# Optimization experiments

Hardware: AMD Instinct MI355X
Metric: run time of the kernel (lower is better)

The kernel has to match this reference:

```python
import jax, jax.numpy as jnp
import numpy as np

B, T, D = 4, 2048, 1024
DEPTH = 4
LEAF_DIM = 256
NUM_LEAVES = 2 ** DEPTH          # 16
NUM_NODES = NUM_LEAVES - 1       # 15


def _uniform(key, shape, scale):
    s = 1.0 / np.sqrt(scale)
    return jax.random.uniform(key, shape, minval=-s, maxval=s, dtype=jnp.float32)


def setup_inputs() -> dict:
    key = jax.random.key(0)
    ks = jax.random.split(key, 8)
    x = jax.random.normal(ks[0], (B, T, D), dtype=jnp.float32)
    # gate params: Dense(1) per internal node, level-order layout
    node_w = _uniform(ks[1], (NUM_NODES, D), D)
    node_b = _uniform(ks[2], (NUM_NODES,), D)
    # leaf MLP params: D -> LEAF_DIM -> D, stacked over leaves
    w1 = _uniform(ks[3], (NUM_LEAVES, D, LEAF_DIM), D)
    b1 = _uniform(ks[4], (NUM_LEAVES, LEAF_DIM), D)
    w2 = _uniform(ks[5], (NUM_LEAVES, LEAF_DIM, D), LEAF_DIM)
    b2 = _uniform(ks[6], (NUM_LEAVES, D), LEAF_DIM)
    return {"x": x, "node_w": node_w, "node_b": node_b,
            "w1": w1, "b1": b1, "w2": w2, "b2": b2, "training": 0}


def _leaf_probs(x, node_w, node_b, depth):
    # gate activations for all internal nodes at once: [B,T,NUM_NODES]
    c = jax.nn.sigmoid(jnp.einsum('btd,nd->btn', x, node_w) + node_b)
    probs = jnp.ones(c.shape[:-1] + (1,), dtype=c.dtype)
    for m in range(depth):
        start = 2 ** m - 1
        cl = c[..., start:start + 2 ** m]          # gates at level m: [B,T,2^m]
        # left child gets c, right child gets (1-c); interleave preserves
        # the recursion's n -> (2n, 2n+1) indexing
        probs = jnp.stack([probs * cl, probs * (1.0 - cl)], axis=-1)
        probs = probs.reshape(probs.shape[:-2] + (-1,))
    return probs                                   # [B,T,NUM_LEAVES]


def reference(x, node_w, node_b, w1, b1, w2, b2, training):
    num_leaves = w1.shape[0]
    depth = int(np.log2(num_leaves))
    probs = _leaf_probs(x, node_w, node_b, depth)          # [B,T,L]
    # all leaf MLP hidden layers as one batched GEMM
    h = jax.nn.relu(jnp.einsum('btd,ldh->btlh', x, w1) + b1)
    # weight hidden by leaf probability, then contract l and h together so the
    # [B,T,L,D] per-leaf output is never materialized
    h = h * probs[..., None]
    out = jnp.einsum('btlh,lhd->btd', h, w2)
    out = out + jnp.einsum('btl,ld->btd', probs, b2)
    return out
```

## Files before the change

kernel.cpp:

```cpp
#include <hip/hip_runtime.h>
#include <stdint.h>

typedef unsigned short ushort_t;
typedef __bf16 bf16x8 __attribute__((ext_vector_type(8)));
typedef float f32x4 __attribute__((ext_vector_type(4)));

#define M_TOK 8192
#define K1 1024
#define N1 4096
#define K2 4160
#define N2 1024

#define SGB(m, n) __builtin_amdgcn_sched_group_barrier((m), (n), 0)
#define SGB_DS   0x100
#define SGB_MFMA 0x008

__device__ __forceinline__ ushort_t f2bf(float f) {
  union { float f; unsigned u; } v; v.f = f;
  unsigned u = v.u;
  u += 0x7FFFu + ((u >> 16) & 1u);
  return (ushort_t)(u >> 16);
}

__device__ __forceinline__ void gload16(const void* g, void* l) {
  __builtin_amdgcn_global_load_lds((__attribute__((address_space(1))) void*)g,
                                   (__attribute__((address_space(3))) void*)l,
                                   16, 0, 0);
}

__global__ __launch_bounds__(256) void k_probs(
    const float* __restrict__ x, const float* __restrict__ node_w,
    const float* __restrict__ node_b, ushort_t* __restrict__ xb,
    float* __restrict__ probs, ushort_t* __restrict__ hp) {
  const int wid = threadIdx.x >> 6, lane = threadIdx.x & 63;
  const int t = blockIdx.x * 4 + wid;
  const float* xr = x + (size_t)t * K1;
  float xv[16];
#pragma unroll
  for (int j = 0; j < 4; ++j) {
    float4 v = *(const float4*)(xr + j * 256 + lane * 4);
    xv[4*j+0] = v.x; xv[4*j+1] = v.y; xv[4*j+2] = v.z; xv[4*j+3] = v.w;
  }
  ushort_t* xbr = xb + (size_t)t * K1;
#pragma unroll
  for (int j = 0; j < 4; ++j) {
    ushort4 o;
    o.x = f2bf(xv[4*j+0]); o.y = f2bf(xv[4*j+1]);
    o.z = f2bf(xv[4*j+2]); o.w = f2bf(xv[4*j+3]);
    *(ushort4*)(xbr + j * 256 + lane * 4) = o;
  }
  float c[15];
#pragma unroll
  for (int n = 0; n < 15; ++n) {
    float s = 0.f;
    const float* wr = node_w + n * K1;
#pragma unroll
    for (int j = 0; j < 4; ++j) {
      float4 w = *(const float4*)(wr + j * 256 + lane * 4);
      s += xv[4*j+0]*w.x + xv[4*j+1]*w.y + xv[4*j+2]*w.z + xv[4*j+3]*w.w;
    }
#pragma unroll
    for (int off = 32; off > 0; off >>= 1) s += __shfl_xor(s, off);
    float z = s + node_b[n];
    c[n] = 1.f / (1.f + __expf(-z));
  }
  if (lane < 16) {
    float p = 1.f;
#pragma unroll
    for (int m = 0; m < 4; ++m) {
      int jm = lane >> (4 - m);
      int node = (1 << m) - 1 + jm;
      int bit = (lane >> (3 - m)) & 1;
      p *= bit ? (1.f - c[node]) : c[node];
    }
    probs[t * 16 + lane] = p;
    hp[(size_t)t * K2 + 4096 + lane] = f2bf(p);
  }
  if (lane < 48) hp[(size_t)t * K2 + 4112 + lane] = 0;
}

__global__ __launch_bounds__(256) void k_wprep(
    const float* __restrict__ w1, const float* __restrict__ w2,
    const float* __restrict__ b2, ushort_t* __restrict__ w1t,
    ushort_t* __restrict__ w2t) {
  __shared__ ushort_t tile[64][68];
  const int b = blockIdx.x;
  const int tr = threadIdx.x >> 4;
  const int tc = (threadIdx.x & 15) * 4;
  if (b < 1024) {
    const int l = b >> 6, rem = b & 63;
    const int kt = rem >> 2, ht = rem & 3;
    const float* in = w1 + (size_t)l * K1 * 256;
#pragma unroll
    for (int rr = 0; rr < 4; ++rr) {
      int r = tr + rr * 16;
      float4 v = *(const float4*)(in + (size_t)(kt * 64 + r) * 256 + ht * 64 + tc);
      tile[r][tc+0] = f2bf(v.x); tile[r][tc+1] = f2bf(v.y);
      tile[r][tc+2] = f2bf(v.z); tile[r][tc+3] = f2bf(v.w);
    }
    __syncthreads();
#pragma unroll
    for (int rr = 0; rr < 4; ++rr) {
      int oh = tr + rr * 16;
      ushort4 o;
      o.x = tile[tc+0][oh]; o.y = tile[tc+1][oh];
      o.z = tile[tc+2][oh]; o.w = tile[tc+3][oh];
      *(ushort4*)(w1t + (size_t)(l * 256 + ht * 64 + oh) * K1 + kt * 64 + tc) = o;
    }
  } else if (b < 2048) {
    const int bb = b - 1024;
    const int l = bb >> 6, rem = bb & 63;
    const int ht = rem >> 4, dt = rem & 15;
    const float* in = w2 + (size_t)l * 256 * N2;
#pragma unroll
    for (int rr = 0; rr < 4; ++rr) {
      int r = tr + rr * 16;
      float4 v = *(const float4*)(in + (size_t)(ht * 64 + r) * N2 + dt * 64 + tc);
      tile[r][tc+0] = f2bf(v.x); tile[r][tc+1] = f2bf(v.y);
      tile[r][tc+2] = f2bf(v.z); tile[r][tc+3] = f2bf(v.w);
    }
    __syncthreads();
#pragma unroll
    for (int rr = 0; rr < 4; ++rr) {
      int od = tr + rr * 16;
      ushort4 o;
      o.x = tile[tc+0][od]; o.y = tile[tc+1][od];
      o.z = tile[tc+2][od]; o.w = tile[tc+3][od];
      *(ushort4*)(w2t + (size_t)(dt * 64 + od) * K2 + l * 256 + ht * 64 + tc) = o;
    }
  } else {
    int tid = (b - 2048) * 256 + threadIdx.x;
    int d = tid >> 6, cc = tid & 63;
    float v = (cc < 16) ? b2[cc * N2 + d] : 0.f;
    w2t[(size_t)d * K2 + 4096 + cc] = f2bf(v);
  }
}

template <int NT, int LDA, int LDB, int BN, int MODE>
__global__ __launch_bounds__(512, 2) void k_gemm8(
    const ushort_t* __restrict__ A, const ushort_t* __restrict__ Bt,
    const float* __restrict__ probs, const float* __restrict__ b1,
    ushort_t* __restrict__ hp, float* __restrict__ out, int ntn) {
  constexpr int BHR = BN / 2;
  constexpr int WN = (BN == 256) ? 4 : 2;
  constexpr int WM = 8 / WN;
  constexpr int FH = 128 / (WM * 16);
  constexpr int ABYTES = 128 * 128;
  constexpr int BBYTES = BHR * 128;
  constexpr int KEEP = 2 + 2 * (BHR / 64);

  extern __shared__ char lds[];
  const int tid = threadIdx.x;
  int bid = blockIdx.x;
  const int nwg = gridDim.x;
  bid = (bid & 7) * (nwg >> 3) + (bid >> 3);
  const int bm = bid / ntn, bn = bid % ntn;

  const int wid = tid >> 6, lane = tid & 63;
  const int widM = wid / WN, widN = wid % WN;
  const int wmBase = widM * (FH * 16);
  const int wn = widN * 64;
  const int lr = lane & 15, g = lane >> 4;

  const ushort_t* Ag = A + (size_t)bm * 256 * LDA;
  const ushort_t* Bg = Bt + (size_t)bn * BN * LDB;

  const int srow = tid >> 3;
  const int scol = ((tid & 7) << 4) ^ ((srow & 7) << 4);

  auto stageA = [&](int buf, int half, int kt) {
    const ushort_t* src = Ag + (size_t)(half * 128) * LDA + kt * 64;
    char* dst = lds + (buf * 2 + half) * ABYTES + tid * 16;
#pragma unroll
    for (int r = 0; r < 2; ++r)
      gload16((const char*)(src + (size_t)(srow + r * 64) * LDA) + scol,
              dst + r * 8192);
  };
  auto stageB = [&](int buf, int half, int kt) {
    const ushort_t* src = Bg + (size_t)(half * BHR) * LDB + kt * 64;
    char* dst = lds + 4 * ABYTES + (buf * 2 + half) * BBYTES + tid * 16;
#pragma unroll
    for (int r = 0; r < BHR / 64; ++r)
      gload16((const char*)(src + (size_t)(srow + r * 64) * LDB) + scol,
              dst + r * 8192);
  };
  auto rdA = [&](int buf, int half, int i, int kk) -> bf16x8 {
    int r = wmBase + i * 16 + lr;
    int off = r * 128 + (((kk * 4 + g) ^ (lr & 7)) << 4);
    return *(const bf16x8*)(lds + (buf * 2 + half) * ABYTES + off);
  };
  auto rdB = [&](int buf, int j, int kk) -> bf16x8 {
    int nr = wn + j * 16;
    int half = (nr >= BHR) ? 1 : 0;
    int r = (nr & (BHR - 1)) + lr;
    int off = r * 128 + (((kk * 4 + g) ^ (lr & 7)) << 4);
    return *(const bf16x8*)(lds + 4 * ABYTES + (buf * 2 + half) * BBYTES + off);
  };

  f32x4 acc[2 * FH][4];
#pragma unroll
  for (int i = 0; i < 2 * FH; ++i)
#pragma unroll
    for (int j = 0; j < 4; ++j) acc[i][j] = (f32x4){0.f, 0.f, 0.f, 0.f};

  stageA(0, 0, 0); stageA(0, 1, 0); stageB(0, 0, 0); stageB(0, 1, 0);
  stageA(1, 0, 1); stageB(1, 0, 1); stageB(1, 1, 1);
  if constexpr (KEEP == 6) asm volatile("s_waitcnt vmcnt(6)" ::: "memory");
  else                     asm volatile("s_waitcnt vmcnt(4)" ::: "memory");
  __builtin_amdgcn_sched_barrier(0);
  __builtin_amdgcn_s_barrier();
  __builtin_amdgcn_sched_barrier(0);

#pragma unroll 1
  for (int kt = 0; kt < NT; ++kt) {
    const int cur = kt & 1;
    bf16x8 bfr[2][4];

    {
      bf16x8 a0[FH][2];
#pragma unroll
      for (int kk = 0; kk < 2; ++kk) {
#pragma unroll
        for (int i = 0; i < FH; ++i) a0[i][kk] = rdA(cur, 0, i, kk);
#pragma unroll
        for (int j = 0; j < 4; ++j) bfr[kk][j] = rdB(cur, j, kk);
      }
      if (kt + 1 < NT) stageA(cur ^ 1, 1, kt + 1);
      __builtin_amdgcn_s_setprio(1);
#pragma unroll
      for (int kk = 0; kk < 2; ++kk)
#pragma unroll
        for (int j = 0; j < 4; ++j)
#pragma unroll
          for (int i = 0; i < FH; ++i)
            acc[i][j] = __builtin_amdgcn_mfma_f32_16x16x32_bf16(
                a0[i][kk], bfr[kk][j], acc[i][j], 0, 0, 0);
      __builtin_amdgcn_s_setprio(0);
#pragma unroll
      for (int kk = 0; kk < 2; ++kk) {
        SGB(SGB_DS, FH + 1); SGB(SGB_MFMA, FH);
#pragma unroll
        for (int rep = 0; rep < 3; ++rep) { SGB(SGB_DS, 1); SGB(SGB_MFMA, FH); }
      }
    }
    __builtin_amdgcn_s_barrier();
    __builtin_amdgcn_sched_barrier(0);

    {
      bf16x8 a1[FH][2];
#pragma unroll
      for (int kk = 0; kk < 2; ++kk)
#pragma unroll
        for (int i = 0; i < FH; ++i) a1[i][kk] = rdA(cur, 1, i, kk);
      if (kt + 2 < NT) {
        stageA(cur, 0, kt + 2);
        stageB(cur, 0, kt + 2);
        stageB(cur, 1, kt + 2);
      }
      __builtin_amdgcn_s_setprio(1);
#pragma unroll
      for (int kk = 0; kk < 2; ++kk)
#pragma unroll
        for (int j = 0; j < 4; ++j)
#pragma unroll
          for (int i = 0; i < FH; ++i)
            acc[FH + i][j] = __builtin_amdgcn_mfma_f32_16x16x32_bf16(
                a1[i][kk], bfr[kk][j], acc[FH + i][j], 0, 0, 0);
      __builtin_amdgcn_s_setprio(0);
#pragma unroll
      for (int kk = 0; kk < 2; ++kk) {
        SGB(SGB_DS, FH); SGB(SGB_MFMA, 2 * FH); SGB(SGB_MFMA, 2 * FH);
      }
    }
    if (kt + 2 < NT) {
      if constexpr (KEEP == 6) asm volatile("s_waitcnt vmcnt(6)" ::: "memory");
      else                     asm volatile("s_waitcnt vmcnt(4)" ::: "memory");
      __builtin_amdgcn_sched_barrier(0);
    } else if (kt + 1 < NT) {
      asm volatile("s_waitcnt vmcnt(0)" ::: "memory");
      __builtin_amdgcn_sched_barrier(0);
    }
    __builtin_amdgcn_s_barrier();
    __builtin_amdgcn_sched_barrier(0);
  }

  const int rowb = bm * 256 + wmBase + g * 4;
  const int colb = bn * BN + wn + lr;
  if (MODE == 0) {
    const int leaf = bn;
#pragma unroll
    for (int q = 0; q < 2; ++q)
#pragma unroll
      for (int i = 0; i < FH; ++i) {
        int rbase = rowb + q * 128 + i * 16;
        float pm[4];
#pragma unroll
        for (int rg = 0; rg < 4; ++rg)
          pm[rg] = probs[(size_t)(rbase + rg) * 16 + leaf];
#pragma unroll
        for (int j = 0; j < 4; ++j) {
          float bias = b1[colb + j * 16];
#pragma unroll
          for (int rg = 0; rg < 4; ++rg) {
            float v = acc[q * FH + i][j][rg] + bias;
            v = v > 0.f ? v : 0.f;
            v *= pm[rg];
            hp[(size_t)(rbase + rg) * K2 + colb + j * 16] = f2bf(v);
          }
        }
      }
  } else {
#pragma unroll
    for (int q = 0; q < 2; ++q)
#pragma unroll
      for (int i = 0; i < FH; ++i) {
        int rbase = rowb + q * 128 + i * 16;
#pragma unroll
        for (int j = 0; j < 4; ++j)
#pragma unroll
          for (int rg = 0; rg < 4; ++rg)
            out[(size_t)(rbase + rg) * N2 + colb + j * 16] = acc[q * FH + i][j][rg];
      }
  }
}

extern "C" void kernel_launch(void* const* d_in, const int* in_sizes, int n_in,
                              void* d_out, int out_size, void* d_ws, size_t ws_size,
                              hipStream_t stream) {
  const float* x      = (const float*)d_in[0];
  const float* node_w = (const float*)d_in[1];
  const float* node_b = (const float*)d_in[2];
  const float* w1     = (const float*)d_in[3];
  const float* b1     = (const float*)d_in[4];
  const float* w2     = (const float*)d_in[5];
  const float* b2     = (const float*)d_in[6];
  float* out = (float*)d_out;

  char* ws = (char*)d_ws;
  ushort_t* xb    = (ushort_t*)(ws);
  ushort_t* w1t   = (ushort_t*)(ws + 16777216);
  ushort_t* w2t   = (ushort_t*)(ws + 25165824);
  ushort_t* hp    = (ushort_t*)(ws + 33685504);
  float*    probs = (float*)   (ws + 101842944);

  k_probs<<<M_TOK / 4, 256, 0, stream>>>(x, node_w, node_b, xb, probs, hp);
  k_wprep<<<2304, 256, 0, stream>>>(w1, w2, b2, w1t, w2t);
  k_gemm8<16, K1, K1, 256, 0><<<512, 512, 131072, stream>>>(
      xb, w1t, probs, b1, hp, nullptr, N1 / 256);
  k_gemm8<65, K2, K2, 128, 1><<<256, 512, 98304, stream>>>(
      hp, w2t, nullptr, nullptr, nullptr, out, N2 / 128);
}
```

Before: 179.3 us.

## Merge prep kernels, unroll GEMM k-loop by two, precompute staging pointers

The gate/probability kernel and the weight-transpose kernel become one launch with a larger grid, removing a kernel launch and its gap. In the GEMM, the per-lane global source pointers are computed once, so each stage only adds an offset. The k-loop is unrolled by two with a compile-time buffer index, which makes LDS offsets constant. The explicit sched_group_barrier interleaving hints are removed, so instruction interleaving is left to the compiler and may get worse.

```diff
diff --git a/kernel.cpp b/kernel.cpp
--- a/kernel.cpp
+++ b/kernel.cpp
@@ -11,9 +11,7 @@
 #define K2 4160
 #define N2 1024
 
-#define SGB(m, n) __builtin_amdgcn_sched_group_barrier((m), (n), 0)
-#define SGB_DS   0x100
-#define SGB_MFMA 0x008
+template <int V> struct ic { static constexpr int value = V; };
 
 __device__ __forceinline__ ushort_t f2bf(float f) {
   union { float f; unsigned u; } v; v.f = f;
@@ -28,66 +26,17 @@
                                    16, 0, 0);
 }
 
-__global__ __launch_bounds__(256) void k_probs(
+__global__ __launch_bounds__(256) void k_prep(
     const float* __restrict__ x, const float* __restrict__ node_w,
-    const float* __restrict__ node_b, ushort_t* __restrict__ xb,
-    float* __restrict__ probs, ushort_t* __restrict__ hp) {
-  const int wid = threadIdx.x >> 6, lane = threadIdx.x & 63;
-  const int t = blockIdx.x * 4 + wid;
-  const float* xr = x + (size_t)t * K1;
-  float xv[16];
-#pragma unroll
-  for (int j = 0; j < 4; ++j) {
-    float4 v = *(const float4*)(xr + j * 256 + lane * 4);
-    xv[4*j+0] = v.x; xv[4*j+1] = v.y; xv[4*j+2] = v.z; xv[4*j+3] = v.w;
-  }
-  ushort_t* xbr = xb + (size_t)t * K1;
-#pragma unroll
-  for (int j = 0; j < 4; ++j) {
-    ushort4 o;
-    o.x = f2bf(xv[4*j+0]); o.y = f2bf(xv[4*j+1]);
-    o.z = f2bf(xv[4*j+2]); o.w = f2bf(xv[4*j+3]);
-    *(ushort4*)(xbr + j * 256 + lane * 4) = o;
-  }
-  float c[15];
-#pragma unroll
-  for (int n = 0; n < 15; ++n) {
-    float s = 0.f;
-    const float* wr = node_w + n * K1;
-#pragma unroll
-    for (int j = 0; j < 4; ++j) {
-      float4 w = *(const float4*)(wr + j * 256 + lane * 4);
-      s += xv[4*j+0]*w.x + xv[4*j+1]*w.y + xv[4*j+2]*w.z + xv[4*j+3]*w.w;
-    }
-#pragma unroll
-    for (int off = 32; off > 0; off >>= 1) s += __shfl_xor(s, off);
-    float z = s + node_b[n];
-    c[n] = 1.f / (1.f + __expf(-z));
-  }
-  if (lane < 16) {
-    float p = 1.f;
-#pragma unroll
-    for (int m = 0; m < 4; ++m) {
-      int jm = lane >> (4 - m);
-      int node = (1 << m) - 1 + jm;
-      int bit = (lane >> (3 - m)) & 1;
-      p *= bit ? (1.f - c[node]) : c[node];
-    }
-    probs[t * 16 + lane] = p;
-    hp[(size_t)t * K2 + 4096 + lane] = f2bf(p);
-  }
-  if (lane < 48) hp[(size_t)t * K2 + 4112 + lane] = 0;
-}
-
-__global__ __launch_bounds__(256) void k_wprep(
-    const float* __restrict__ w1, const float* __restrict__ w2,
-    const float* __restrict__ b2, ushort_t* __restrict__ w1t,
-    ushort_t* __restrict__ w2t) {
+    const float* __restrict__ node_b, const float* __restrict__ w1,
+    const float* __restrict__ w2, const float* __restrict__ b2,
+    ushort_t* __restrict__ xb, float* __restrict__ probs,
+    ushort_t* __restrict__ w1t, ushort_t* __restrict__ w2t,
+    ushort_t* __restrict__ hp) {
   __shared__ ushort_t tile[64][68];
   const int b = blockIdx.x;
-  const int tr = threadIdx.x >> 4;
-  const int tc = (threadIdx.x & 15) * 4;
   if (b < 1024) {
+    const int tr = threadIdx.x >> 4, tc = (threadIdx.x & 15) * 4;
     const int l = b >> 6, rem = b & 63;
     const int kt = rem >> 2, ht = rem & 3;
     const float* in = w1 + (size_t)l * K1 * 256;
@@ -108,6 +57,7 @@
       *(ushort4*)(w1t + (size_t)(l * 256 + ht * 64 + oh) * K1 + kt * 64 + tc) = o;
     }
   } else if (b < 2048) {
+    const int tr = threadIdx.x >> 4, tc = (threadIdx.x & 15) * 4;
     const int bb = b - 1024;
     const int l = bb >> 6, rem = bb & 63;
     const int ht = rem >> 4, dt = rem & 15;
@@ -128,11 +78,57 @@
       o.z = tile[tc+2][od]; o.w = tile[tc+3][od];
       *(ushort4*)(w2t + (size_t)(dt * 64 + od) * K2 + l * 256 + ht * 64 + tc) = o;
     }
-  } else {
+  } else if (b < 2304) {
     int tid = (b - 2048) * 256 + threadIdx.x;
     int d = tid >> 6, cc = tid & 63;
     float v = (cc < 16) ? b2[cc * N2 + d] : 0.f;
     w2t[(size_t)d * K2 + 4096 + cc] = f2bf(v);
+  } else {
+    const int wid = threadIdx.x >> 6, lane = threadIdx.x & 63;
+    const int t = (b - 2304) * 4 + wid;
+    const float* xr = x + (size_t)t * K1;
+    float xv[16];
+#pragma unroll
+    for (int j = 0; j < 4; ++j) {
+      float4 v = *(const float4*)(xr + j * 256 + lane * 4);
+      xv[4*j+0] = v.x; xv[4*j+1] = v.y; xv[4*j+2] = v.z; xv[4*j+3] = v.w;
+    }
+    ushort_t* xbr = xb + (size_t)t * K1;
+#pragma unroll
+    for (int j = 0; j < 4; ++j) {
+      ushort4 o;
+      o.x = f2bf(xv[4*j+0]); o.y = f2bf(xv[4*j+1]);
+      o.z = f2bf(xv[4*j+2]); o.w = f2bf(xv[4*j+3]);
+      *(ushort4*)(xbr + j * 256 + lane * 4) = o;
+    }
+    float c[15];
+#pragma unroll
+    for (int n = 0; n < 15; ++n) {
+      float s = 0.f;
+      const float* wr = node_w + n * K1;
+#pragma unroll
+      for (int j = 0; j < 4; ++j) {
+        float4 w = *(const float4*)(wr + j * 256 + lane * 4);
+        s += xv[4*j+0]*w.x + xv[4*j+1]*w.y + xv[4*j+2]*w.z + xv[4*j+3]*w.w;
+      }
+#pragma unroll
+      for (int off = 32; off > 0; off >>= 1) s += __shfl_xor(s, off);
+      float z = s + node_b[n];
+      c[n] = 1.f / (1.f + __expf(-z));
+    }
+    if (lane < 16) {
+      float p = 1.f;
+#pragma unroll
+      for (int m = 0; m < 4; ++m) {
+        int jm = lane >> (4 - m);
+        int node = (1 << m) - 1 + jm;
+        int bit = (lane >> (3 - m)) & 1;
+        p *= bit ? (1.f - c[node]) : c[node];
+      }
+      probs[t * 16 + lane] = p;
+      hp[(size_t)t * K2 + 4096 + lane] = f2bf(p);
+    }
+    if (lane < 48) hp[(size_t)t * K2 + 4112 + lane] = 0;
   }
 }
 
@@ -168,21 +164,22 @@
   const int srow = tid >> 3;
   const int scol = ((tid & 7) << 4) ^ ((srow & 7) << 4);
 
+  const char* pA = (const char*)(Ag + (size_t)srow * LDA) + scol;
+  const char* pB = (const char*)(Bg + (size_t)srow * LDB) + scol;
+
   auto stageA = [&](int buf, int half, int kt) {
-    const ushort_t* src = Ag + (size_t)(half * 128) * LDA + kt * 64;
+    const char* src = pA + (size_t)(half * 128) * (LDA * 2) + kt * 128;
     char* dst = lds + (buf * 2 + half) * ABYTES + tid * 16;
 #pragma unroll
     for (int r = 0; r < 2; ++r)
-      gload16((const char*)(src + (size_t)(srow + r * 64) * LDA) + scol,
-              dst + r * 8192);
+      gload16(src + (size_t)(r * 64) * (LDA * 2), dst + r * 8192);
   };
   auto stageB = [&](int buf, int half, int kt) {
-    const ushort_t* src = Bg + (size_t)(half * BHR) * LDB + kt * 64;
+    const char* src = pB + (size_t)(half * BHR) * (LDB * 2) + kt * 128;
     char* dst = lds + 4 * ABYTES + (buf * 2 + half) * BBYTES + tid * 16;
 #pragma unroll
     for (int r = 0; r < BHR / 64; ++r)
-      gload16((const char*)(src + (size_t)(srow + r * 64) * LDB) + scol,
-              dst + r * 8192);
+      gload16(src + (size_t)(r * 64) * (LDB * 2), dst + r * 8192);
   };
   auto rdA = [&](int buf, int half, int i, int kk) -> bf16x8 {
     int r = wmBase + i * 16 + lr;
@@ -211,11 +208,9 @@
   __builtin_amdgcn_s_barrier();
   __builtin_amdgcn_sched_barrier(0);
 
-#pragma unroll 1
-  for (int kt = 0; kt < NT; ++kt) {
-    const int cur = kt & 1;
+  auto body = [&](auto CURC, int kt) {
+    constexpr int cur = decltype(CURC)::value;
     bf16x8 bfr[2][4];
-
     {
       bf16x8 a0[FH][2];
 #pragma unroll
@@ -236,16 +231,9 @@
             acc[i][j] = __builtin_amdgcn_mfma_f32_16x16x32_bf16(
                 a0[i][kk], bfr[kk][j], acc[i][j], 0, 0, 0);
       __builtin_amdgcn_s_setprio(0);
-#pragma unroll
-      for (int kk = 0; kk < 2; ++kk) {
-        SGB(SGB_DS, FH + 1); SGB(SGB_MFMA, FH);
-#pragma unroll
-        for (int rep = 0; rep < 3; ++rep) { SGB(SGB_DS, 1); SGB(SGB_MFMA, FH); }
-      }
     }
     __builtin_amdgcn_s_barrier();
     __builtin_amdgcn_sched_barrier(0);
-
     {
       bf16x8 a1[FH][2];
 #pragma unroll
@@ -267,10 +255,6 @@
             acc[FH + i][j] = __builtin_amdgcn_mfma_f32_16x16x32_bf16(
                 a1[i][kk], bfr[kk][j], acc[FH + i][j], 0, 0, 0);
       __builtin_amdgcn_s_setprio(0);
-#pragma unroll
-      for (int kk = 0; kk < 2; ++kk) {
-        SGB(SGB_DS, FH); SGB(SGB_MFMA, 2 * FH); SGB(SGB_MFMA, 2 * FH);
-      }
     }
     if (kt + 2 < NT) {
       if constexpr (KEEP == 6) asm volatile("s_waitcnt vmcnt(6)" ::: "memory");
@@ -282,7 +266,15 @@
     }
     __builtin_amdgcn_s_barrier();
     __builtin_amdgcn_sched_barrier(0);
+  };
+
+  int kt = 0;
+#pragma unroll 1
+  for (int it = 0; it < NT / 2; ++it) {
+    body(ic<0>{}, kt); ++kt;
+    body(ic<1>{}, kt); ++kt;
   }
+  if constexpr (NT & 1) body(ic<0>{}, kt);
 
   const int rowb = bm * 256 + wmBase + g * 4;
   const int colb = bn * BN + wn + lr;
@@ -343,8 +335,8 @@
   ushort_t* hp    = (ushort_t*)(ws + 33685504);
   float*    probs = (float*)   (ws + 101842944);
 
-  k_probs<<<M_TOK / 4, 256, 0, stream>>>(x, node_w, node_b, xb, probs, hp);
-  k_wprep<<<2304, 256, 0, stream>>>(w1, w2, b2, w1t, w2t);
+  k_prep<<<4352, 256, 0, stream>>>(x, node_w, node_b, w1, w2, b2,
+                                   xb, probs, w1t, w2t, hp);
   k_gemm8<16, K1, K1, 256, 0><<<512, 512, 131072, stream>>>(
       xb, w1t, probs, b1, hp, nullptr, N1 / 256);
   k_gemm8<65, K2, K2, 128, 1><<<256, 512, 98304, stream>>>(
```

Result: faster. 169.0 us (median of 3 runs) (-5.7%).
